# Performance work log

Hardware: AMD Instinct MI355X
Metric: run time of the kernel (lower is better)

Reference implementation:

```python
import jax, jax.numpy as jnp
import numpy as np


def setup_inputs() -> dict:
    key = jax.random.key(0)
    ks = jax.random.split(key, 5)
    N, C, H, W = 4, 256, 64, 64
    fan_scale = 1.0 / np.sqrt(C)  # kaiming-ish scale for 1x1 conv weights
    x = jax.random.normal(ks[0], (N, C, H, W), dtype=jnp.float32)
    Wq = jax.random.normal(ks[1], (C, C), dtype=jnp.float32) * fan_scale
    Wk = jax.random.normal(ks[2], (C, C), dtype=jnp.float32) * fan_scale
    Wv = jax.random.normal(ks[3], (C, C), dtype=jnp.float32) * fan_scale
    bq = jnp.zeros((C,), dtype=jnp.float32)
    bk = jnp.zeros((C,), dtype=jnp.float32)
    bv = jnp.zeros((C,), dtype=jnp.float32)
    gamma = jax.random.uniform(ks[4], (1,), dtype=jnp.float32)
    return {"x": x, "Wq": Wq, "bq": bq, "Wk": Wk, "bk": bk, "Wv": Wv, "bv": bv, "gamma": gamma}


def reference(x, Wq, bq, Wk, bk, Wv, bv, gamma):
    # x: (N, C, H, W); 1x1 convs are channel-mixing matmuls.
    N, C, H, W = x.shape
    HW = H * W
    xf = x.reshape(N, C, HW)
    q = jnp.einsum('oc,ncl->nol', Wq, xf) + bq[None, :, None]  # (N, C, HW)
    k = jnp.einsum('oc,ncl->nol', Wk, xf) + bk[None, :, None]
    v = jnp.einsum('oc,ncl->nol', Wv, xf) + bv[None, :, None]
    # spatial mode: energy = softmax(Q^T K) over last dim (no 1/sqrt(d) scaling)
    energy = jax.nn.softmax(jnp.einsum('nci,ncj->nij', q, k), axis=-1)  # (N, HW, HW)
    # att[n,c,i] = sum_j v[n,c,j] * energy[n,i,j]  (bmm(value, energy^T))
    att = jnp.einsum('ncj,nij->nci', v, energy)  # (N, C, HW)
    # in_channels == out_channels -> residual is identity
    out = x + gamma[0] * att.reshape(N, C, H, W)
    return out
```

## Files before the change

kernel.cpp:

```cpp
#include <hip/hip_runtime.h>

typedef unsigned short ushort_t;
typedef unsigned int u32;
typedef _Float16 f16;
typedef f16 f16x8 __attribute__((ext_vector_type(8)));
typedef f16 f16x2 __attribute__((ext_vector_type(2)));
typedef ushort_t u16x8 __attribute__((ext_vector_type(8)));
typedef float f32x4 __attribute__((ext_vector_type(4)));

#define C_DIM 256
#define HW 4096
#define CHW (C_DIM*HW)
#define L2E 1.4426950408889634f

__device__ __align__(16) f16 g_xbT[4 * CHW];
__device__ __align__(16) f16 g_q[4 * CHW];
__device__ __align__(16) f16 g_k[4 * CHW];
__device__ __align__(16) f16 g_v[4 * CHW];
__device__ __align__(16) f16 g_opart[16 * CHW];
__device__ __align__(16) float g_ml[16 * 2 * HW];

__device__ __forceinline__ float bf2f(ushort_t h) {
    union { u32 u; float f; } v; v.u = ((u32)h) << 16; return v.f;
}
__device__ __forceinline__ ushort_t f2bf(float f) {
    union { float f; u32 u; } v; v.f = f;
    u32 r = v.u + 0x7FFF + ((v.u >> 16) & 1);
    return (ushort_t)(r >> 16);
}
__device__ __forceinline__ float fin0(float v) {
    return (v > -1e30f && v < 1e30f) ? v : 0.f;
}
__device__ __forceinline__ f16 sf16(float v) {
    return (f16)((v > -1e4f && v < 1e4f) ? v : 0.f);
}
__device__ __forceinline__ void gl2lds16(const f16* g, f16* l) {
    __builtin_amdgcn_global_load_lds(
        (const __attribute__((address_space(1))) u32*)g,
        (__attribute__((address_space(3))) u32*)l, 16, 0, 0);
}
__device__ __forceinline__ int probe_mode(const void* p) {
    int lane = threadIdx.x & 63;
    float v = fabsf(bf2f(((const ushort_t*)p)[lane]));
    v = (v < 1e6f) ? v : 1e6f;
#pragma unroll
    for (int d = 1; d < 64; d <<= 1) v += __shfl_xor(v, d, 64);
    return (v * (1.f / 64.f) > 100.f) ? 1 : 0;
}

__global__ void k_sentinel(ushort_t* out, int n) {
    int i = blockIdx.x * 256 + threadIdx.x;
    if (i < n) out[i] = f2bf(777.f);
}

__global__ __launch_bounds__(256) void k_transpose(const void* __restrict__ xv) {
    __shared__ f16 t[64][66];
    int mode = probe_mode(xv);
    int n = blockIdx.z, c0 = blockIdx.y * 64, l0 = blockIdx.x * 64;
    int tid = threadIdx.x;
    f16* ob = g_xbT + n * CHW;
    int lq = (tid & 15) * 4;
    int cl = tid >> 4;
    if (mode == 0) {
        const ushort_t* xb = (const ushort_t*)xv + n * CHW;
#pragma unroll
        for (int p = 0; p < 4; ++p) {
            int c = cl + 16 * p;
            ushort4 v = *(const ushort4*)(xb + (c0 + c) * HW + l0 + lq);
            t[lq + 0][c] = sf16(bf2f(v.x));
            t[lq + 1][c] = sf16(bf2f(v.y));
            t[lq + 2][c] = sf16(bf2f(v.z));
            t[lq + 3][c] = sf16(bf2f(v.w));
        }
    } else {
        const float* xb = (const float*)xv + n * CHW;
#pragma unroll
        for (int p = 0; p < 4; ++p) {
            int c = cl + 16 * p;
            float4 v = *(const float4*)(xb + (c0 + c) * HW + l0 + lq);
            t[lq + 0][c] = sf16(v.x);
            t[lq + 1][c] = sf16(v.y);
            t[lq + 2][c] = sf16(v.z);
            t[lq + 3][c] = sf16(v.w);
        }
    }
    __syncthreads();
    int c2 = (tid & 31) * 2;
    int lr = tid >> 5;
#pragma unroll
    for (int p = 0; p < 8; ++p) {
        int l = lr + 8 * p;
        u32 pair = *(const u32*)&t[l][c2];
        *(u32*)(ob + (l0 + l) * C_DIM + c0 + c2) = pair;
    }
}

__global__ __launch_bounds__(256) void k_proj(
    const void* __restrict__ Wq, const void* __restrict__ bq,
    const void* __restrict__ Wk, const void* __restrict__ bk,
    const void* __restrict__ Wv, const void* __restrict__ bv)
{
    __shared__ __align__(16) f16 lds_x[128 * 64];
    __shared__ __align__(16) f16 lds_w[128 * 64];
    int l0 = blockIdx.x * 128;
    int og0 = blockIdx.y * 128;
    int n = blockIdx.z;
    int mat = og0 >> 8;
    int om0 = og0 & 255;
    const void* W = (mat == 0) ? Wq : (mat == 1) ? Wk : Wv;
    const void* bias = (mat == 0) ? bq : (mat == 1) ? bk : bv;
    int mode = probe_mode(W);
    int tid = threadIdx.x, w = tid >> 6, lane = tid & 63;
    int quad = lane >> 4, l16 = lane & 15;
    const f16* xb = g_xbT + n * CHW;

    f32x4 acc[2][8];
#pragma unroll
    for (int a = 0; a < 2; a++)
#pragma unroll
        for (int b = 0; b < 8; b++) acc[a][b] = f32x4{0.f, 0.f, 0.f, 0.f};

    for (int ch = 0; ch < 4; ++ch) {
        int cc0 = ch * 64;
        f16x8 xs[4], wsr[4];
#pragma unroll
        for (int ti = 0; ti < 4; ++ti) {
            int s = (w * 4 + ti) * 64 + lane;
            int row = s >> 3, gp = s & 7;
            xs[ti] = *(const f16x8*)(xb + (l0 + row) * C_DIM + cc0 + gp * 8);
            f16x8 h;
            if (mode == 0) {
                u16x8 wv = *(const u16x8*)((const ushort_t*)W + (om0 + row) * C_DIM + cc0 + gp * 8);
#pragma unroll
                for (int e = 0; e < 8; e++) h[e] = sf16(bf2f(wv[e]));
            } else {
                const float* wf = (const float*)W + (om0 + row) * C_DIM + cc0 + gp * 8;
#pragma unroll
                for (int e = 0; e < 8; e++) h[e] = sf16(wf[e]);
            }
            wsr[ti] = h;
        }
        __syncthreads();
#pragma unroll
        for (int ti = 0; ti < 4; ++ti) {
            int s = (w * 4 + ti) * 64 + lane;
            int row = s >> 3, gp = s & 7;
            int pos = gp ^ (row & 7);
            *(f16x8*)(lds_x + (row * 8 + pos) * 8) = xs[ti];
            *(f16x8*)(lds_w + (row * 8 + pos) * 8) = wsr[ti];
        }
        __syncthreads();
#pragma unroll
        for (int ks = 0; ks < 2; ++ks) {
            f16x8 af[2];
#pragma unroll
            for (int mt = 0; mt < 2; ++mt) {
                int row = w * 32 + mt * 16 + l16;
                int g = ks * 4 + quad;
                int pos = g ^ (row & 7);
                af[mt] = *(const f16x8*)(lds_x + (row * 8 + pos) * 8);
            }
#pragma unroll
            for (int nt = 0; nt < 8; ++nt) {
                int rowo = nt * 16 + l16;
                int g = ks * 4 + quad;
                int pos = g ^ (rowo & 7);
                f16x8 bfv = *(const f16x8*)(lds_w + (rowo * 8 + pos) * 8);
                if (mat < 2) {
                    acc[0][nt] = __builtin_amdgcn_mfma_f32_16x16x32_f16(af[0], bfv, acc[0][nt], 0, 0, 0);
                    acc[1][nt] = __builtin_amdgcn_mfma_f32_16x16x32_f16(af[1], bfv, acc[1][nt], 0, 0, 0);
                } else {
                    acc[0][nt] = __builtin_amdgcn_mfma_f32_16x16x32_f16(bfv, af[0], acc[0][nt], 0, 0, 0);
                    acc[1][nt] = __builtin_amdgcn_mfma_f32_16x16x32_f16(bfv, af[1], acc[1][nt], 0, 0, 0);
                }
            }
        }
        __syncthreads();
    }

    auto loadb = [&](int i) -> float {
        return mode ? ((const float*)bias)[i] : bf2f(((const ushort_t*)bias)[i]);
    };
    if (mat < 2) {
        f16* T = ((mat == 0) ? g_q : g_k) + n * CHW;
        float bvv[8];
#pragma unroll
        for (int nt = 0; nt < 8; nt++) bvv[nt] = loadb(om0 + nt * 16 + l16);
#pragma unroll
        for (int mt = 0; mt < 2; mt++)
#pragma unroll
            for (int nt = 0; nt < 8; nt++)
#pragma unroll
                for (int r = 0; r < 4; r++) {
                    int l = l0 + w * 32 + mt * 16 + quad * 4 + r;
                    int o = om0 + nt * 16 + l16;
                    T[l * C_DIM + o] = sf16(acc[mt][nt][r] + bvv[nt]);
                }
    } else {
        f16* T = g_v + n * CHW;
#pragma unroll
        for (int mt = 0; mt < 2; mt++)
#pragma unroll
            for (int nt = 0; nt < 8; nt++)
#pragma unroll
                for (int r = 0; r < 4; r++) {
                    int o = om0 + nt * 16 + quad * 4 + r;
                    int l = l0 + w * 32 + mt * 16 + l16;
                    T[o * HW + l] = sf16(acc[mt][nt][r] + loadb(o));
                }
    }
}

__global__ __launch_bounds__(256, 2) void k_attn() {
    __shared__ __align__(16) char smem[70656];
    f16* kbuf = (f16*)smem;
    f16* vbuf = (f16*)(smem + 32768);
    f16* pb   = (f16*)(smem + 65536);

    int bid = blockIdx.x;
    int x8 = bid & 7;
    int n = x8 >> 1, jhi = x8 & 1;
    int rest = bid >> 3;
    int jlo = rest & 1;
    int i0 = (rest >> 1) * 128;
    int jq = jhi * 2 + jlo;
    int tid = threadIdx.x, w = tid >> 6, lane = tid & 63;
    int quad = lane >> 4, l16 = lane & 15;

    const f16* Qb = g_q + n * CHW;
    const f16* Kb = g_k + n * CHW;
    const f16* Vb = g_v + n * CHW;
    f16* pw = pb + w * 640;

    int koff0[8], koff1[8], voff[16];
#pragma unroll
    for (int kk = 0; kk < 8; kk++) {
        int g2 = kk * 4 + quad;
        int pos = (g2 & 24) | ((g2 & 7) ^ (l16 & 7));
        koff0[kk] = (l16 * 32 + pos) * 8;
        koff1[kk] = ((16 + l16) * 32 + pos) * 8;
    }
#pragma unroll
    for (int ct = 0; ct < 16; ct++) {
        int c = ct * 16 + l16;
        voff[ct] = (c * 4 + (quad ^ ((c >> 1) & 3))) * 8;
    }

    f16x8 qf[2][8];
#pragma unroll
    for (int mt = 0; mt < 2; mt++) {
        const f16* qrow = Qb + (i0 + w * 32 + mt * 16 + l16) * C_DIM + quad * 8;
#pragma unroll
        for (int kk = 0; kk < 8; kk++)
            qf[mt][kk] = *(const f16x8*)(qrow + kk * 32);
    }

    f32x4 o_acc[2][16];
#pragma unroll
    for (int mt = 0; mt < 2; mt++)
#pragma unroll
        for (int i = 0; i < 16; i++) o_acc[mt][i] = f32x4{0.f, 0.f, 0.f, 0.f};
    float m_[2] = {-1e30f, -1e30f}, l_[2] = {0.f, 0.f};

    auto stageK = [&](int jt, int buf) {
#pragma unroll
        for (int s = 0; s < 4; ++s) {
            int idx = s * 256 + tid;
            int j = idx >> 5, gp = idx & 31;
            int gg = (gp & 24) | ((gp & 7) ^ (j & 7));
            gl2lds16(Kb + (jt * 32 + j) * C_DIM + gg * 8,
                     kbuf + (buf * 1024 + s * 256 + w * 64) * 8);
        }
    };
    auto stageV = [&](int jt, int buf) {
#pragma unroll
        for (int s = 0; s < 4; ++s) {
            int idx = s * 256 + tid;
            int c = idx >> 2, jp = idx & 3;
            int jg = jp ^ ((c >> 1) & 3);
            gl2lds16(Vb + c * HW + jt * 32 + jg * 8,
                     vbuf + (buf * 1024 + s * 256 + w * 64) * 8);
        }
    };

    int jt0 = jq * 32;
    stageK(jt0, 0);
    stageV(jt0, 0);
    __syncthreads();

    for (int it = 0; it < 32; ++it) {
        int buf = it & 1;
        if (it + 1 < 32) {
            stageK(jt0 + it + 1, buf ^ 1);
            stageV(jt0 + it + 1, buf ^ 1);
        }

        const f16* kb = kbuf + buf * 8192;
        const f16* vb = vbuf + buf * 8192;

        f32x4 st[2][2];
        st[0][0] = f32x4{0.f,0.f,0.f,0.f}; st[0][1] = f32x4{0.f,0.f,0.f,0.f};
        st[1][0] = f32x4{0.f,0.f,0.f,0.f}; st[1][1] = f32x4{0.f,0.f,0.f,0.f};
#pragma unroll
        for (int kk = 0; kk < 8; kk++) {
            f16x8 kf0 = *(const f16x8*)(kb + koff0[kk]);
            f16x8 kf1 = *(const f16x8*)(kb + koff1[kk]);
            st[0][0] = __builtin_amdgcn_mfma_f32_16x16x32_f16(kf0, qf[0][kk], st[0][0], 0, 0, 0);
            st[0][1] = __builtin_amdgcn_mfma_f32_16x16x32_f16(kf1, qf[0][kk], st[0][1], 0, 0, 0);
            st[1][0] = __builtin_amdgcn_mfma_f32_16x16x32_f16(kf0, qf[1][kk], st[1][0], 0, 0, 0);
            st[1][1] = __builtin_amdgcn_mfma_f32_16x16x32_f16(kf1, qf[1][kk], st[1][1], 0, 0, 0);
        }

        float al[2];
        float pv0[2][4], pv1[2][4];
#pragma unroll
        for (int mt = 0; mt < 2; mt++) {
            float smax = fmaxf(fmaxf(fmaxf(st[mt][0][0], st[mt][0][1]), fmaxf(st[mt][0][2], st[mt][0][3])),
                               fmaxf(fmaxf(st[mt][1][0], st[mt][1][1]), fmaxf(st[mt][1][2], st[mt][1][3])));
            smax = fmaxf(smax, __shfl_xor(smax, 16, 64));
            smax = fmaxf(smax, __shfl_xor(smax, 32, 64));
            float mq = __builtin_ceilf(smax * 0.125f) * 8.f;
            float mn = fmaxf(m_[mt], mq);
            al[mt] = __builtin_amdgcn_exp2f((m_[mt] - mn) * L2E);
            float rs = 0.f;
#pragma unroll
            for (int r = 0; r < 4; r++) {
                pv0[mt][r] = __builtin_amdgcn_exp2f((st[mt][0][r] - mn) * L2E);
                pv1[mt][r] = __builtin_amdgcn_exp2f((st[mt][1][r] - mn) * L2E);
                rs += pv0[mt][r] + pv1[mt][r];
            }
            m_[mt] = mn;
            rs += __shfl_xor(rs, 16, 64);
            rs += __shfl_xor(rs, 32, 64);
            l_[mt] = l_[mt] * al[mt] + rs;
        }
        if (__any((al[0] < 1.0f) || (al[1] < 1.0f))) {
#pragma unroll
            for (int mt = 0; mt < 2; mt++)
#pragma unroll
                for (int t = 0; t < 16; t++) o_acc[mt][t] *= al[mt];
        }

        f16* pm = pw + l16 * 40;
        *(f16x2*)(pm + quad * 4)          = f16x2{(f16)pv0[0][0], (f16)pv0[0][1]};
        *(f16x2*)(pm + quad * 4 + 2)      = f16x2{(f16)pv0[0][2], (f16)pv0[0][3]};
        *(f16x2*)(pm + 16 + quad * 4)     = f16x2{(f16)pv1[0][0], (f16)pv1[0][1]};
        *(f16x2*)(pm + 16 + quad * 4 + 2) = f16x2{(f16)pv1[0][2], (f16)pv1[0][3]};
        asm volatile("" ::: "memory");
        f16x8 pf0 = *(const f16x8*)(pw + l16 * 40 + quad * 8);
        asm volatile("" ::: "memory");
        *(f16x2*)(pm + quad * 4)          = f16x2{(f16)pv0[1][0], (f16)pv0[1][1]};
        *(f16x2*)(pm + quad * 4 + 2)      = f16x2{(f16)pv0[1][2], (f16)pv0[1][3]};
        *(f16x2*)(pm + 16 + quad * 4)     = f16x2{(f16)pv1[1][0], (f16)pv1[1][1]};
        *(f16x2*)(pm + 16 + quad * 4 + 2) = f16x2{(f16)pv1[1][2], (f16)pv1[1][3]};
        asm volatile("" ::: "memory");
        f16x8 pf1 = *(const f16x8*)(pw + l16 * 40 + quad * 8);

#pragma unroll
        for (int ct = 0; ct < 16; ++ct) {
            f16x8 vf = *(const f16x8*)(vb + voff[ct]);
            o_acc[0][ct] = __builtin_amdgcn_mfma_f32_16x16x32_f16(vf, pf0, o_acc[0][ct], 0, 0, 0);
            o_acc[1][ct] = __builtin_amdgcn_mfma_f32_16x16x32_f16(vf, pf1, o_acc[1][ct], 0, 0, 0);
        }

        __syncthreads();
    }

    int slot = jq * 4 + n;
    if (quad == 0) {
#pragma unroll
        for (int mt = 0; mt < 2; mt++) {
            int i = i0 + w * 32 + mt * 16 + l16;
            g_ml[(slot * 2 + 0) * HW + i] = m_[mt];
            g_ml[(slot * 2 + 1) * HW + i] = l_[mt];
        }
    }
    f16* ob = g_opart + slot * CHW;
    int ig0 = i0 + w * 32 + l16;
    float inv0 = (l_[0] > 1e-30f) ? 1.0f / l_[0] : 0.f;
    float inv1 = (l_[1] > 1e-30f) ? 1.0f / l_[1] : 0.f;
#pragma unroll
    for (int ct = 0; ct < 16; ct++)
#pragma unroll
        for (int r = 0; r < 4; r++) {
            int c = ct * 16 + quad * 4 + r;
            ob[c * HW + ig0]      = (f16)(o_acc[0][ct][r] * inv0);
            ob[c * HW + ig0 + 16] = (f16)(o_acc[1][ct][r] * inv1);
        }
}

__global__ __launch_bounds__(256) void k_combine(
    const void* __restrict__ xv, const void* __restrict__ gv, void* __restrict__ outv)
{
    int mode = probe_mode(xv);
    float gam = fin0(mode ? ((const float*)gv)[0] : bf2f(((const ushort_t*)gv)[0]));
    int n = blockIdx.y;
    int off = blockIdx.x * 2048 + threadIdx.x * 8;
    int i = off & (HW - 1);

    u16x8 op[4];
    float ms[4][8], ls[4][8];
#pragma unroll
    for (int s = 0; s < 4; ++s) {
        int slot = s * 4 + n;
        op[s] = *(const u16x8*)((const ushort_t*)g_opart + slot * CHW + off);
        float4 mA = *(const float4*)&g_ml[(slot * 2 + 0) * HW + i];
        float4 mB = *(const float4*)&g_ml[(slot * 2 + 0) * HW + i + 4];
        float4 lA = *(const float4*)&g_ml[(slot * 2 + 1) * HW + i];
        float4 lB = *(const float4*)&g_ml[(slot * 2 + 1) * HW + i + 4];
        ms[s][0]=mA.x; ms[s][1]=mA.y; ms[s][2]=mA.z; ms[s][3]=mA.w;
        ms[s][4]=mB.x; ms[s][5]=mB.y; ms[s][6]=mB.z; ms[s][7]=mB.w;
        ls[s][0]=lA.x; ls[s][1]=lA.y; ls[s][2]=lA.z; ls[s][3]=lA.w;
        ls[s][4]=lB.x; ls[s][5]=lB.y; ls[s][6]=lB.z; ls[s][7]=lB.w;
    }

    float o[8];
#pragma unroll
    for (int e = 0; e < 8; ++e) {
        float m = fmaxf(fmaxf(ms[0][e], ms[1][e]), fmaxf(ms[2][e], ms[3][e]));
        float num = 0.f, den = 0.f;
#pragma unroll
        for (int s = 0; s < 4; ++s) {
            float wgt = __builtin_amdgcn_exp2f((ms[s][e] - m) * L2E) * ls[s][e];
            union { ushort_t u; f16 h; } cv; cv.u = (ushort_t)op[s][e];
            num += wgt * (float)cv.h;
            den += wgt;
        }
        o[e] = (den > 1e-30f) ? num / den : 0.f;
    }

    if (mode == 0) {
        u16x8 xp = *(const u16x8*)((const ushort_t*)xv + n * CHW + off);
        u16x8 res;
#pragma unroll
        for (int e = 0; e < 8; ++e)
            res[e] = f2bf(fin0(bf2f((ushort_t)xp[e]) + gam * o[e]));
        *(u16x8*)((ushort_t*)outv + n * CHW + off) = res;
    } else {
        const float* xb = (const float*)xv + n * CHW + off;
        float* outb = (float*)outv + n * CHW + off;
        float4 xA = *(const float4*)xb;
        float4 xB = *(const float4*)(xb + 4);
        float4 rA, rB;
        rA.x = fin0(xA.x + gam * o[0]); rA.y = fin0(xA.y + gam * o[1]);
        rA.z = fin0(xA.z + gam * o[2]); rA.w = fin0(xA.w + gam * o[3]);
        rB.x = fin0(xB.x + gam * o[4]); rB.y = fin0(xB.y + gam * o[5]);
        rB.z = fin0(xB.z + gam * o[6]); rB.w = fin0(xB.w + gam * o[7]);
        *(float4*)outb = rA;
        *(float4*)(outb + 4) = rB;
    }
}

extern "C" void kernel_launch(void* const* d_in, const int* in_sizes, int n_in,
                              void* d_out, int out_size, void* d_ws, size_t ws_size,
                              hipStream_t stream) {
    (void)d_ws; (void)ws_size;
    bool ok = (n_in == 8) &&
              in_sizes[0] == 4 * CHW &&
              in_sizes[1] == C_DIM * C_DIM && in_sizes[2] == C_DIM &&
              in_sizes[3] == C_DIM * C_DIM && in_sizes[4] == C_DIM &&
              in_sizes[5] == C_DIM * C_DIM && in_sizes[6] == C_DIM &&
              in_sizes[7] == 1 && out_size == 4 * CHW;
    if (!ok) {
        hipLaunchKernelGGL(k_sentinel, dim3((out_size + 255) / 256), dim3(256), 0, stream,
                           (ushort_t*)d_out, out_size);
        return;
    }
    hipLaunchKernelGGL(k_transpose, dim3(64, 4, 4), dim3(256), 0, stream, d_in[0]);
    hipLaunchKernelGGL(k_proj, dim3(32, 6, 4), dim3(256), 0, stream,
                       d_in[1], d_in[2], d_in[3], d_in[4], d_in[5], d_in[6]);
    hipLaunchKernelGGL(k_attn, dim3(512), dim3(256), 0, stream);
    hipLaunchKernelGGL(k_combine, dim3(CHW / 2048, 4), dim3(256), 0, stream,
                       d_in[0], d_in[7], d_out);
}
```

Baseline: 234.9 us.

## Rewrite attention loop with 32x32 MFMA, register P shuffle, and skewed PV pipeline

Measured after the change: 239.9 us. 1.02x slower.

```diff
diff --git a/kernel.cpp b/kernel.cpp
--- a/kernel.cpp
+++ b/kernel.cpp
@@ -7,6 +7,7 @@
 typedef f16 f16x2 __attribute__((ext_vector_type(2)));
 typedef ushort_t u16x8 __attribute__((ext_vector_type(8)));
 typedef float f32x4 __attribute__((ext_vector_type(4)));
+typedef float f32x16 __attribute__((ext_vector_type(16)));
 
 #define C_DIM 256
 #define HW 4096
@@ -211,11 +212,28 @@
     }
 }
 
+__device__ __forceinline__ f16x8 pack_pfrag(const float* p, int h) {
+    union PK { u32 u; f16x2 h2; } t0, t1, t2, t3;
+    t0.h2 = f16x2{(f16)p[0], (f16)p[1]};
+    t1.h2 = f16x2{(f16)p[2], (f16)p[3]};
+    t2.h2 = f16x2{(f16)p[4], (f16)p[5]};
+    t3.h2 = f16x2{(f16)p[6], (f16)p[7]};
+    u32 sa = __shfl_xor(t0.u, 32, 64);
+    u32 sb = __shfl_xor(t1.u, 32, 64);
+    u32 sc = __shfl_xor(t2.u, 32, 64);
+    u32 sd = __shfl_xor(t3.u, 32, 64);
+    union RW { u32 w[4]; f16x8 v; } r;
+    r.w[0] = h ? sc : t0.u;
+    r.w[1] = h ? sd : t1.u;
+    r.w[2] = h ? t2.u : sa;
+    r.w[3] = h ? t3.u : sb;
+    return r.v;
+}
+
 __global__ __launch_bounds__(256, 2) void k_attn() {
-    __shared__ __align__(16) char smem[70656];
-    f16* kbuf = (f16*)smem;
-    f16* vbuf = (f16*)(smem + 32768);
-    f16* pb   = (f16*)(smem + 65536);
+    __shared__ __align__(16) f16 smem[40960];
+    f16* kbuf = smem;
+    f16* vbuf = smem + 16384;
 
     int bid = blockIdx.x;
     int x8 = bid & 7;
@@ -225,168 +243,152 @@
     int i0 = (rest >> 1) * 128;
     int jq = jhi * 2 + jlo;
     int tid = threadIdx.x, w = tid >> 6, lane = tid & 63;
-    int quad = lane >> 4, l16 = lane & 15;
+    int j5 = lane & 31, h = lane >> 5;
 
     const f16* Qb = g_q + n * CHW;
     const f16* Kb = g_k + n * CHW;
     const f16* Vb = g_v + n * CHW;
-    f16* pw = pb + w * 640;
-
-    int koff0[8], koff1[8], voff[16];
-#pragma unroll
-    for (int kk = 0; kk < 8; kk++) {
-        int g2 = kk * 4 + quad;
-        int pos = (g2 & 24) | ((g2 & 7) ^ (l16 & 7));
-        koff0[kk] = (l16 * 32 + pos) * 8;
-        koff1[kk] = ((16 + l16) * 32 + pos) * 8;
-    }
-#pragma unroll
-    for (int ct = 0; ct < 16; ct++) {
-        int c = ct * 16 + l16;
-        voff[ct] = (c * 4 + (quad ^ ((c >> 1) & 3))) * 8;
-    }
-
-    f16x8 qf[2][8];
-#pragma unroll
-    for (int mt = 0; mt < 2; mt++) {
-        const f16* qrow = Qb + (i0 + w * 32 + mt * 16 + l16) * C_DIM + quad * 8;
-#pragma unroll
-        for (int kk = 0; kk < 8; kk++)
-            qf[mt][kk] = *(const f16x8*)(qrow + kk * 32);
-    }
-
-    f32x4 o_acc[2][16];
-#pragma unroll
-    for (int mt = 0; mt < 2; mt++)
-#pragma unroll
-        for (int i = 0; i < 16; i++) o_acc[mt][i] = f32x4{0.f, 0.f, 0.f, 0.f};
-    float m_[2] = {-1e30f, -1e30f}, l_[2] = {0.f, 0.f};
-
-    auto stageK = [&](int jt, int buf) {
-#pragma unroll
-        for (int s = 0; s < 4; ++s) {
-            int idx = s * 256 + tid;
-            int j = idx >> 5, gp = idx & 31;
-            int gg = (gp & 24) | ((gp & 7) ^ (j & 7));
-            gl2lds16(Kb + (jt * 32 + j) * C_DIM + gg * 8,
-                     kbuf + (buf * 1024 + s * 256 + w * 64) * 8);
-        }
-    };
-    auto stageV = [&](int jt, int buf) {
-#pragma unroll
-        for (int s = 0; s < 4; ++s) {
-            int idx = s * 256 + tid;
-            int c = idx >> 2, jp = idx & 3;
-            int jg = jp ^ ((c >> 1) & 3);
-            gl2lds16(Vb + c * HW + jt * 32 + jg * 8,
-                     vbuf + (buf * 1024 + s * 256 + w * 64) * 8);
-        }
-    };
-
-    int jt0 = jq * 32;
-    stageK(jt0, 0);
-    stageV(jt0, 0);
+
+    f16x8 qf[16];
+    {
+        const f16* qrow = Qb + (i0 + w * 32 + j5) * C_DIM + h * 8;
+#pragma unroll
+        for (int ck = 0; ck < 16; ++ck)
+            qf[ck] = *(const f16x8*)(qrow + ck * 16);
+    }
+
+    int k_lane = h * 256 + j5 * 8;
+    int v_lane = h * 2048 + j5 * 8;
+
+    const f16* ksrc = Kb + (jq * 1024 + j5) * C_DIM + (w * 2 + h) * 8;
+    const f16* vsrc = Vb + tid * HW + jq * 1024;
+    int dst_w = w * 512;
+
+    f32x16 o_acc[8];
+#pragma unroll
+    for (int ct = 0; ct < 8; ++ct)
+#pragma unroll
+        for (int r = 0; r < 16; ++r) o_acc[ct][r] = 0.f;
+
+    float m_ = -1e30f, l_ = 0.f, al_prev = 1.f;
+    f16x8 pf0 = {}, pf1 = {};
+
+#pragma unroll
+    for (int s = 0; s < 4; ++s) gl2lds16(ksrc + s * 64, kbuf + s * 2048 + dst_w);
+    ksrc += 32 * C_DIM;
+#pragma unroll
+    for (int s = 0; s < 4; ++s) gl2lds16(vsrc + s * 8, vbuf + s * 2048 + dst_w);
+    vsrc += 32;
     __syncthreads();
 
+    int vs_stage = 1, vs_pv = 2;
     for (int it = 0; it < 32; ++it) {
-        int buf = it & 1;
-        if (it + 1 < 32) {
-            stageK(jt0 + it + 1, buf ^ 1);
-            stageV(jt0 + it + 1, buf ^ 1);
-        }
-
-        const f16* kb = kbuf + buf * 8192;
-        const f16* vb = vbuf + buf * 8192;
-
-        f32x4 st[2][2];
-        st[0][0] = f32x4{0.f,0.f,0.f,0.f}; st[0][1] = f32x4{0.f,0.f,0.f,0.f};
-        st[1][0] = f32x4{0.f,0.f,0.f,0.f}; st[1][1] = f32x4{0.f,0.f,0.f,0.f};
-#pragma unroll
-        for (int kk = 0; kk < 8; kk++) {
-            f16x8 kf0 = *(const f16x8*)(kb + koff0[kk]);
-            f16x8 kf1 = *(const f16x8*)(kb + koff1[kk]);
-            st[0][0] = __builtin_amdgcn_mfma_f32_16x16x32_f16(kf0, qf[0][kk], st[0][0], 0, 0, 0);
-            st[0][1] = __builtin_amdgcn_mfma_f32_16x16x32_f16(kf1, qf[0][kk], st[0][1], 0, 0, 0);
-            st[1][0] = __builtin_amdgcn_mfma_f32_16x16x32_f16(kf0, qf[1][kk], st[1][0], 0, 0, 0);
-            st[1][1] = __builtin_amdgcn_mfma_f32_16x16x32_f16(kf1, qf[1][kk], st[1][1], 0, 0, 0);
-        }
-
-        float al[2];
-        float pv0[2][4], pv1[2][4];
-#pragma unroll
-        for (int mt = 0; mt < 2; mt++) {
-            float smax = fmaxf(fmaxf(fmaxf(st[mt][0][0], st[mt][0][1]), fmaxf(st[mt][0][2], st[mt][0][3])),
-                               fmaxf(fmaxf(st[mt][1][0], st[mt][1][1]), fmaxf(st[mt][1][2], st[mt][1][3])));
-            smax = fmaxf(smax, __shfl_xor(smax, 16, 64));
-            smax = fmaxf(smax, __shfl_xor(smax, 32, 64));
-            float mq = __builtin_ceilf(smax * 0.125f) * 8.f;
-            float mn = fmaxf(m_[mt], mq);
-            al[mt] = __builtin_amdgcn_exp2f((m_[mt] - mn) * L2E);
-            float rs = 0.f;
-#pragma unroll
-            for (int r = 0; r < 4; r++) {
-                pv0[mt][r] = __builtin_amdgcn_exp2f((st[mt][0][r] - mn) * L2E);
-                pv1[mt][r] = __builtin_amdgcn_exp2f((st[mt][1][r] - mn) * L2E);
-                rs += pv0[mt][r] + pv1[mt][r];
+        int kb_cur = it & 1;
+        if (it < 31) {
+#pragma unroll
+            for (int s = 0; s < 4; ++s)
+                gl2lds16(ksrc + s * 64, kbuf + (kb_cur ^ 1) * 8192 + s * 2048 + dst_w);
+            ksrc += 32 * C_DIM;
+#pragma unroll
+            for (int s = 0; s < 4; ++s)
+                gl2lds16(vsrc + s * 8, vbuf + vs_stage * 8192 + s * 2048 + dst_w);
+            vsrc += 32;
+        }
+
+        const f16* kb = kbuf + kb_cur * 8192 + k_lane;
+        f32x16 st;
+#pragma unroll
+        for (int r = 0; r < 16; ++r) st[r] = 0.f;
+        __builtin_amdgcn_s_setprio(1);
+#pragma unroll
+        for (int ck = 0; ck < 16; ++ck) {
+            f16x8 kf = *(const f16x8*)(kb + ck * 512);
+            st = __builtin_amdgcn_mfma_f32_32x32x16_f16(kf, qf[ck], st, 0, 0, 0);
+        }
+
+        if (it > 0) {
+            if (__any(al_prev < 1.f)) {
+#pragma unroll
+                for (int ct = 0; ct < 8; ++ct)
+#pragma unroll
+                    for (int r = 0; r < 16; ++r) o_acc[ct][r] *= al_prev;
             }
-            m_[mt] = mn;
-            rs += __shfl_xor(rs, 16, 64);
-            rs += __shfl_xor(rs, 32, 64);
-            l_[mt] = l_[mt] * al[mt] + rs;
-        }
-        if (__any((al[0] < 1.0f) || (al[1] < 1.0f))) {
-#pragma unroll
-            for (int mt = 0; mt < 2; mt++)
-#pragma unroll
-                for (int t = 0; t < 16; t++) o_acc[mt][t] *= al[mt];
-        }
-
-        f16* pm = pw + l16 * 40;
-        *(f16x2*)(pm + quad * 4)          = f16x2{(f16)pv0[0][0], (f16)pv0[0][1]};
-        *(f16x2*)(pm + quad * 4 + 2)      = f16x2{(f16)pv0[0][2], (f16)pv0[0][3]};
-        *(f16x2*)(pm + 16 + quad * 4)     = f16x2{(f16)pv1[0][0], (f16)pv1[0][1]};
-        *(f16x2*)(pm + 16 + quad * 4 + 2) = f16x2{(f16)pv1[0][2], (f16)pv1[0][3]};
-        asm volatile("" ::: "memory");
-        f16x8 pf0 = *(const f16x8*)(pw + l16 * 40 + quad * 8);
-        asm volatile("" ::: "memory");
-        *(f16x2*)(pm + quad * 4)          = f16x2{(f16)pv0[1][0], (f16)pv0[1][1]};
-        *(f16x2*)(pm + quad * 4 + 2)      = f16x2{(f16)pv0[1][2], (f16)pv0[1][3]};
-        *(f16x2*)(pm + 16 + quad * 4)     = f16x2{(f16)pv1[1][0], (f16)pv1[1][1]};
-        *(f16x2*)(pm + 16 + quad * 4 + 2) = f16x2{(f16)pv1[1][2], (f16)pv1[1][3]};
-        asm volatile("" ::: "memory");
-        f16x8 pf1 = *(const f16x8*)(pw + l16 * 40 + quad * 8);
-
-#pragma unroll
-        for (int ct = 0; ct < 16; ++ct) {
-            f16x8 vf = *(const f16x8*)(vb + voff[ct]);
-            o_acc[0][ct] = __builtin_amdgcn_mfma_f32_16x16x32_f16(vf, pf0, o_acc[0][ct], 0, 0, 0);
-            o_acc[1][ct] = __builtin_amdgcn_mfma_f32_16x16x32_f16(vf, pf1, o_acc[1][ct], 0, 0, 0);
-        }
+            const f16* vb = vbuf + vs_pv * 8192 + v_lane;
+#pragma unroll
+            for (int ct = 0; ct < 8; ++ct) {
+                f16x8 v0 = *(const f16x8*)(vb + ct * 256);
+                f16x8 v1 = *(const f16x8*)(vb + 4096 + ct * 256);
+                o_acc[ct] = __builtin_amdgcn_mfma_f32_32x32x16_f16(v0, pf0, o_acc[ct], 0, 0, 0);
+                o_acc[ct] = __builtin_amdgcn_mfma_f32_32x32x16_f16(v1, pf1, o_acc[ct], 0, 0, 0);
+            }
+        }
+        __builtin_amdgcn_s_setprio(0);
+
+        float mx0 = fmaxf(fmaxf(st[0], st[1]), fmaxf(st[2], st[3]));
+        float mx1 = fmaxf(fmaxf(st[4], st[5]), fmaxf(st[6], st[7]));
+        float mx2 = fmaxf(fmaxf(st[8], st[9]), fmaxf(st[10], st[11]));
+        float mx3 = fmaxf(fmaxf(st[12], st[13]), fmaxf(st[14], st[15]));
+        float smax = fmaxf(fmaxf(mx0, mx1), fmaxf(mx2, mx3));
+        smax = fmaxf(smax, __shfl_xor(smax, 32, 64));
+        float mq = __builtin_ceilf(smax * 0.125f) * 8.f;
+        float mn = fmaxf(m_, mq);
+        float al = __builtin_amdgcn_exp2f((m_ - mn) * L2E);
+        float nl = -mn * L2E;
+        float p[16];
+#pragma unroll
+        for (int r = 0; r < 16; ++r)
+            p[r] = __builtin_amdgcn_exp2f(st[r] * L2E + nl);
+        float a0 = (p[0] + p[1]) + (p[2] + p[3]);
+        float a1 = (p[4] + p[5]) + (p[6] + p[7]);
+        float a2 = (p[8] + p[9]) + (p[10] + p[11]);
+        float a3 = (p[12] + p[13]) + (p[14] + p[15]);
+        float rs = (a0 + a1) + (a2 + a3);
+        rs += __shfl_xor(rs, 32, 64);
+        m_ = mn;
+        l_ = l_ * al + rs;
+        al_prev = al;
+        pf0 = pack_pfrag(p, h);
+        pf1 = pack_pfrag(p + 8, h);
 
         __syncthreads();
+        vs_pv = (vs_pv == 2) ? 0 : vs_pv + 1;
+        vs_stage = (vs_stage == 2) ? 0 : vs_stage + 1;
+    }
+
+    {
+        if (__any(al_prev < 1.f)) {
+#pragma unroll
+            for (int ct = 0; ct < 8; ++ct)
+#pragma unroll
+                for (int r = 0; r < 16; ++r) o_acc[ct][r] *= al_prev;
+        }
+        const f16* vb = vbuf + vs_pv * 8192 + v_lane;
+#pragma unroll
+        for (int ct = 0; ct < 8; ++ct) {
+            f16x8 v0 = *(const f16x8*)(vb + ct * 256);
+            f16x8 v1 = *(const f16x8*)(vb + 4096 + ct * 256);
+            o_acc[ct] = __builtin_amdgcn_mfma_f32_32x32x16_f16(v0, pf0, o_acc[ct], 0, 0, 0);
+            o_acc[ct] = __builtin_amdgcn_mfma_f32_32x32x16_f16(v1, pf1, o_acc[ct], 0, 0, 0);
+        }
     }
 
     int slot = jq * 4 + n;
-    if (quad == 0) {
-#pragma unroll
-        for (int mt = 0; mt < 2; mt++) {
-            int i = i0 + w * 32 + mt * 16 + l16;
-            g_ml[(slot * 2 + 0) * HW + i] = m_[mt];
-            g_ml[(slot * 2 + 1) * HW + i] = l_[mt];
-        }
-    }
-    f16* ob = g_opart + slot * CHW;
-    int ig0 = i0 + w * 32 + l16;
-    float inv0 = (l_[0] > 1e-30f) ? 1.0f / l_[0] : 0.f;
-    float inv1 = (l_[1] > 1e-30f) ? 1.0f / l_[1] : 0.f;
-#pragma unroll
-    for (int ct = 0; ct < 16; ct++)
-#pragma unroll
-        for (int r = 0; r < 4; r++) {
-            int c = ct * 16 + quad * 4 + r;
-            ob[c * HW + ig0]      = (f16)(o_acc[0][ct][r] * inv0);
-            ob[c * HW + ig0 + 16] = (f16)(o_acc[1][ct][r] * inv1);
-        }
+    int i_out = i0 + w * 32 + j5;
+    if (h == 0) {
+        g_ml[(slot * 2 + 0) * HW + i_out] = m_;
+        g_ml[(slot * 2 + 1) * HW + i_out] = l_;
+    }
+    float inv = (l_ > 1e-30f) ? 1.f / l_ : 0.f;
+    f16* ob = g_opart + slot * CHW + i_out;
+#pragma unroll
+    for (int ct = 0; ct < 8; ++ct) {
+        int cbase = ct * 32 + 4 * h;
+#pragma unroll
+        for (int r = 0; r < 16; ++r) {
+            int c = cbase + (r & 3) + 8 * (r >> 2);
+            ob[c * HW] = (f16)(o_acc[ct][r] * inv);
+        }
+    }
 }
 
 __global__ __launch_bounds__(256) void k_combine(
```
